# Kernel tuning notes

Measured on AMD Instinct MI355X. Metric: run time of the kernel, lower is better.

The kernel has to match this reference:

```python
import jax, jax.numpy as jnp
import numpy as np

B, T, S = 4, 2048, 512
HID, ND, NH = 2048, 1024, 16
HD = HID // NH  # 128
GATING_INIT = -4.0


def setup_inputs() -> dict:
    key = jax.random.key(0)
    ks = jax.random.split(key, 12)
    sc_h = 1.0 / np.sqrt(HID)
    sc_n = 1.0 / np.sqrt(ND)
    mask = jax.random.bernoulli(ks[2], 0.9, (B, S))
    mask = mask.at[:, 0].set(True)  # avoid fully-masked rows (NaN softmax)
    return {
        "hidden_states": jax.random.normal(ks[0], (B, T, HID), jnp.float32),
        "notes": jax.random.normal(ks[1], (B, S, ND), jnp.float32),
        "notes_mask": mask,
        "q_w": jax.random.normal(ks[3], (HID, HID), jnp.float32) * sc_h,
        "q_b": jax.random.normal(ks[4], (HID,), jnp.float32) * 0.01,
        "k_w": jax.random.normal(ks[5], (HID, ND), jnp.float32) * sc_n,
        "k_b": jax.random.normal(ks[6], (HID,), jnp.float32) * 0.01,
        "v_w": jax.random.normal(ks[7], (HID, ND), jnp.float32) * sc_n,
        "v_b": jax.random.normal(ks[8], (HID,), jnp.float32) * 0.01,
        "o_w": jax.random.normal(ks[9], (HID, HID), jnp.float32) * sc_h,
        "o_b": jax.random.normal(ks[10], (HID,), jnp.float32) * 0.01,
        "gate": jnp.full((1,), GATING_INIT, jnp.float32),
    }


def reference(hidden_states, notes, notes_mask, q_w, q_b, k_w, k_b, v_w, v_b, o_w, o_b, gate):
    # projections (torch Linear: x @ W^T + b)
    q = hidden_states @ q_w.T + q_b            # (B,T,HID)
    k = notes @ k_w.T + k_b                    # (B,S,HID)
    v = notes @ v_w.T + v_b                    # (B,S,HID)
    q = q.reshape(B, T, NH, HD).transpose(0, 2, 1, 3)  # (B,H,T,D)
    k = k.reshape(B, S, NH, HD).transpose(0, 2, 1, 3)  # (B,H,S,D)
    v = v.reshape(B, S, NH, HD).transpose(0, 2, 1, 3)
    scores = jnp.einsum("bhtd,bhsd->bhts", q, k) / jnp.sqrt(jnp.float32(HD))
    scores = jnp.where(notes_mask[:, None, None, :], scores, -jnp.inf)
    attn = jax.nn.softmax(scores, axis=-1)
    context = jnp.einsum("bhts,bhsd->bhtd", attn, v)   # (B,H,T,D)
    g = jax.nn.sigmoid(gate).reshape(1, 1, 1, 1)
    context = (g * context).transpose(0, 2, 1, 3).reshape(B, T, HID)
    delta = context @ o_w.T + o_b
    return delta
```

## Files before the change

kernel.cpp:

```cpp
#include <hip/hip_runtime.h>
#include <hip/hip_bf16.h>
#include <stdint.h>

#define B_ 4
#define T_ 2048
#define S_ 512
#define HID_ 2048
#define ND_ 1024
#define NH_ 16
#define HD_ 128

typedef unsigned short u16;
typedef unsigned int u32;
typedef __attribute__((ext_vector_type(8))) short bf16x8;
typedef __attribute__((ext_vector_type(4))) float f32x4;
typedef __attribute__((ext_vector_type(16))) float f32x16;
typedef __attribute__((ext_vector_type(4))) float f4;
typedef __attribute__((ext_vector_type(4))) u16 us4;
typedef __attribute__((ext_vector_type(8))) u16 us8;
typedef __attribute__((ext_vector_type(4))) u32 u32x4;

__device__ inline u16 f2bf(float f) {
  unsigned u = __builtin_bit_cast(unsigned, f);
  u += 0x7FFFu + ((u >> 16) & 1u);
  return (u16)(u >> 16);
}

__device__ inline u32 cvtpk(float lo, float hi) {
  u32 r;
  asm("v_cvt_pk_bf16_f32 %0, %1, %2" : "=v"(r) : "v"(lo), "v"(hi));
  return r;
}

__device__ inline f32x4 mfma16(bf16x8 a, bf16x8 b, f32x4 c) {
  return __builtin_amdgcn_mfma_f32_16x16x32_bf16(a, b, c, 0, 0, 0);
}
__device__ inline f32x16 mfma32(bf16x8 a, bf16x8 b, f32x16 c) {
  return __builtin_amdgcn_mfma_f32_32x32x16_bf16(a, b, c, 0, 0, 0);
}

__device__ inline void gload_lds16(const u16* g, u16* l) {
  __builtin_amdgcn_global_load_lds(
      (const __attribute__((address_space(1))) unsigned int*)g,
      (__attribute__((address_space(3))) unsigned int*)l, 16, 0, 0);
}

__global__ __launch_bounds__(256) void convert_all(
    const float* __restrict__ h, const float* __restrict__ n,
    const float* __restrict__ qw, const float* __restrict__ kw,
    const float* __restrict__ vw, const float* __restrict__ ow,
    u16* __restrict__ dh, u16* __restrict__ dn, u16* __restrict__ dqw,
    u16* __restrict__ dkw, u16* __restrict__ dvw, u16* __restrict__ dow) {
  const int C0 = 4194304;
  const int C1 = C0 + 524288;
  const int C2 = C1 + 1048576;
  const int C3 = C2 + 524288;
  const int C4 = C3 + 524288;
  const int C5 = C4 + 1048576;
  for (int c = blockIdx.x * blockDim.x + threadIdx.x; c < C5;
       c += gridDim.x * blockDim.x) {
    const float* s; u16* d; int o;
    if (c < C0)      { s = h;  d = dh;  o = c; }
    else if (c < C1) { s = n;  d = dn;  o = c - C0; }
    else if (c < C2) { s = qw; d = dqw; o = c - C1; }
    else if (c < C3) { s = kw; d = dkw; o = c - C2; }
    else if (c < C4) { s = vw; d = dvw; o = c - C3; }
    else             { s = ow; d = dow; o = c - C4; }
    f4 v = ((const f4*)s)[o];
    us4 r = { f2bf(v[0]), f2bf(v[1]), f2bf(v[2]), f2bf(v[3]) };
    ((us4*)d)[o] = r;
  }
}

template <bool OUT_BF16>
__global__ __launch_bounds__(256) void gemm_bt(
    const u16* __restrict__ A, const u16* __restrict__ Bm,
    const float* __restrict__ bias, void* __restrict__ Cout,
    int M, int N, int K) {
  __shared__ u16 As[128 * 32];
  __shared__ u16 Bs[128 * 32];
  const int tid = threadIdx.x;
  const int lane = tid & 63;
  const int wave = tid >> 6;
  const int wr = (wave >> 1) * 64;
  const int wc = (wave & 1) * 64;
  const int c15 = lane & 15;
  const int g = lane >> 4;
  const int bx = blockIdx.x, by = blockIdx.y;

  const u16* gA = A + (size_t)(by * 128 + (tid >> 2)) * K + (tid & 3) * 8;
  const u16* gB = Bm + (size_t)(bx * 128 + (tid >> 2)) * K + (tid & 3) * 8;

  f32x4 acc[4][4];
#pragma unroll
  for (int i = 0; i < 4; ++i)
#pragma unroll
    for (int j = 0; j < 4; ++j) acc[i][j] = (f32x4){0.f, 0.f, 0.f, 0.f};

  for (int k0 = 0; k0 < K; k0 += 32) {
    gload_lds16(gA + k0, &As[wave * 512]);
    gload_lds16(gA + (size_t)64 * K + k0, &As[2048 + wave * 512]);
    gload_lds16(gB + k0, &Bs[wave * 512]);
    gload_lds16(gB + (size_t)64 * K + k0, &Bs[2048 + wave * 512]);
    __syncthreads();
    bf16x8 af[4], bfr[4];
#pragma unroll
    for (int mt = 0; mt < 4; ++mt)
      af[mt] = *(const bf16x8*)&As[(wr + mt * 16 + c15) * 32 + g * 8];
#pragma unroll
    for (int nt = 0; nt < 4; ++nt)
      bfr[nt] = *(const bf16x8*)&Bs[(wc + nt * 16 + c15) * 32 + g * 8];
#pragma unroll
    for (int mt = 0; mt < 4; ++mt)
#pragma unroll
      for (int nt = 0; nt < 4; ++nt)
        acc[mt][nt] = mfma16(af[mt], bfr[nt], acc[mt][nt]);
    __syncthreads();
  }

#pragma unroll
  for (int mt = 0; mt < 4; ++mt)
#pragma unroll
    for (int nt = 0; nt < 4; ++nt) {
      const int m = by * 128 + wr + mt * 16 + g * 4;
      const int n = bx * 128 + wc + nt * 16 + c15;
      const float bv = bias[n];
#pragma unroll
      for (int r = 0; r < 4; ++r) {
        const float v = acc[mt][nt][r] + bv;
        if (OUT_BF16)
          ((u16*)Cout)[(size_t)(m + r) * N + n] = f2bf(v);
        else
          ((float*)Cout)[(size_t)(m + r) * N + n] = v;
      }
    }
}

template <bool OUT_BF16>
__global__ __launch_bounds__(512, 2) void gemm_pipe(
    const u16* __restrict__ A, const u16* __restrict__ Bm,
    const float* __restrict__ bias, void* __restrict__ Cout,
    int M, int N, int K) {
  extern __shared__ u16 lds[];
  const int tid = threadIdx.x;
  const int lane = tid & 63, wave = tid >> 6;
  const int wm = wave >> 2, wn = wave & 3;
  const int c15 = lane & 15, g = lane >> 4;
  const int bid = blockIdx.y * gridDim.x + blockIdx.x;
  const int sw = (bid & 7) * 32 + (bid >> 3);
  const int bn = sw & 7, bm = sw >> 3;
  const int NT = K >> 5;

  const int srow = tid >> 2;
  const int sx = (tid & 3) ^ ((srow >> 1) & 3);
  const u16* pa0 = A + (size_t)(bm * 256 + srow) * K + sx * 8;
  const u16* pa1 = A + (size_t)(bm * 256 + 128 + srow) * K + sx * 8;
  const u16* pb0 = Bm + (size_t)(bn * 256 + srow) * K + sx * 8;
  const u16* pb1 = Bm + (size_t)(bn * 256 + 128 + srow) * K + sx * 8;

  const int xr = (c15 >> 1) & 3;
  const int aoff = wm * 4096 + c15 * 32 + (g ^ xr) * 8;
  const int boff = 8192 + wn * 2048 + c15 * 32 + (g ^ xr) * 8;

  f32x4 acc[8][4];
#pragma unroll
  for (int i = 0; i < 8; ++i)
#pragma unroll
    for (int j = 0; j < 4; ++j) acc[i][j] = (f32x4){0.f, 0.f, 0.f, 0.f};

  {
    u16* sA = lds + wave * 512;
    u16* sB = lds + 8192 + wave * 512;
    gload_lds16(pa0, sA);          gload_lds16(pa1, sA + 4096);
    gload_lds16(pb0, sB);          gload_lds16(pb1, sB + 4096);
    pa0 += 32; pa1 += 32; pb0 += 32; pb1 += 32;
    gload_lds16(pa0, sA + 16384);  gload_lds16(pa1, sA + 20480);
    gload_lds16(pb0, sB + 16384);  gload_lds16(pb1, sB + 20480);
    pa0 += 32; pa1 += 32; pb0 += 32; pb1 += 32;
  }
  asm volatile("s_waitcnt vmcnt(4)" ::: "memory");
  __builtin_amdgcn_s_barrier();

  for (int t = 0; t < NT; ++t) {
    const bool more = (t + 2 < NT);
    const u16* cb = lds + (t & 3) * 16384;
    u16* sb = lds + ((t + 2) & 3) * 16384;

    bf16x8 a[8], b[4];
#pragma unroll
    for (int mf = 0; mf < 4; ++mf)
      a[mf] = *(const bf16x8*)(cb + aoff + mf * 512);
#pragma unroll
    for (int nf = 0; nf < 4; ++nf)
      b[nf] = *(const bf16x8*)(cb + boff + nf * 512);
#pragma unroll
    for (int mf = 4; mf < 8; ++mf)
      a[mf] = *(const bf16x8*)(cb + aoff + mf * 512);

    if (more) {
      gload_lds16(pa0, sb + wave * 512);
      gload_lds16(pa1, sb + 4096 + wave * 512);
      gload_lds16(pb0, sb + 8192 + wave * 512);
      gload_lds16(pb1, sb + 12288 + wave * 512);
      pa0 += 32; pa1 += 32; pb0 += 32; pb1 += 32;
    }

    __builtin_amdgcn_s_setprio(1);
#pragma unroll
    for (int mf = 0; mf < 8; ++mf)
#pragma unroll
      for (int nf = 0; nf < 4; ++nf)
        acc[mf][nf] = mfma16(a[mf], b[nf], acc[mf][nf]);
    __builtin_amdgcn_s_setprio(0);

    if (more) asm volatile("s_waitcnt vmcnt(4)" ::: "memory");
    else      asm volatile("s_waitcnt vmcnt(0)" ::: "memory");
    __builtin_amdgcn_s_barrier();
  }

#pragma unroll
  for (int mf = 0; mf < 8; ++mf)
#pragma unroll
    for (int nf = 0; nf < 4; ++nf) {
      const int m = bm * 256 + wm * 128 + mf * 16 + g * 4;
      const int n = bn * 256 + wn * 64 + nf * 16 + c15;
      const float bv = bias[n];
#pragma unroll
      for (int r = 0; r < 4; ++r) {
        const float v = acc[mf][nf][r] + bv;
        if (OUT_BF16)
          ((u16*)Cout)[(size_t)(m + r) * N + n] = f2bf(v);
        else
          ((float*)Cout)[(size_t)(m + r) * N + n] = v;
      }
    }
}

__global__ __launch_bounds__(256) void transpose_v(const u16* __restrict__ v,
                                                   u16* __restrict__ vt) {
  __shared__ u16 tile[32][36];
  const int s0 = blockIdx.x * 32;
  const int bh = blockIdx.y;
  const int d0 = blockIdx.z * 32;
  const int b = bh >> 4, h = bh & 15;
  const int tid = threadIdx.x;
  const int sl = tid >> 3, dl = (tid & 7) * 4;
  us4 val = *(const us4*)(v + (size_t)(b * S_ + s0 + sl) * HID_ + h * HD_ + d0 + dl);
  *(us4*)&tile[sl][dl] = val;
  __syncthreads();
  const int dl2 = tid >> 3, sl2 = (tid & 7) * 4;
  us4 outv = { tile[sl2 + 0][dl2], tile[sl2 + 1][dl2],
               tile[sl2 + 2][dl2], tile[sl2 + 3][dl2] };
  *(us4*)(vt + ((size_t)bh * HD_ + d0 + dl2) * S_ + s0 + sl2) = outv;
}

__global__ __launch_bounds__(256) void attn_fwd(
    const u16* __restrict__ q, const u16* __restrict__ k,
    const u16* __restrict__ vt, const int* __restrict__ mask,
    const float* __restrict__ gate, u16* __restrict__ ctx) {
  __shared__ u16 smem[17408];
  __shared__ float addend[S_];
  const int tid = threadIdx.x, lane = tid & 63, wave = tid >> 6;
  const int bh = blockIdx.y, b = bh >> 4, h = bh & 15;
  const int tw = blockIdx.x * 128 + wave * 32;
  const int l31 = lane & 31, hi = lane >> 5;

  const u16* kb  = k + (size_t)b * S_ * HID_ + h * HD_;
  const u16* vtb = vt + (size_t)bh * HD_ * S_;

  const u16* sp[4];
  int dj[4];
  u16* ldsbase;
  ptrdiff_t stride;
  if (wave < 2) {
    ldsbase = smem;
    stride = 32 * HID_;
#pragma unroll
    for (int i = 0; i < 4; ++i) {
      const int jj = wave * 4 + i;
      const int row = jj * 4 + (lane >> 4);
      const int cb = (lane & 15) * 16;
      const int cbp = cb ^ ((row & 7) << 4);
      sp[i] = kb + (size_t)row * HID_ + (cbp >> 1);
      dj[i] = jj * 512;
    }
  } else {
    ldsbase = smem + 8192;
    stride = 32;
#pragma unroll
    for (int i = 0; i < 4; ++i) {
      const int jj = (wave - 2) * 4 + i;
      const int d = jj * 16 + (lane >> 2);
      const int cb = (lane & 3) * 16;
      const int cbp = cb ^ ((d & 3) << 4);
      sp[i] = vtb + (size_t)d * S_ + (cbp >> 1);
      dj[i] = jj * 512;
    }
  }
#define STAGE(cur)                                            \
  do {                                                        \
    _Pragma("unroll") for (int i_ = 0; i_ < 4; ++i_) {        \
      gload_lds16(sp[i_], ldsbase + (cur) * 4096 + dj[i_]);   \
      sp[i_] += stride;                                       \
    }                                                         \
  } while (0)

  STAGE(0);

  for (int s = tid; s < S_; s += 256)
    addend[s] = mask[b * S_ + s] ? 0.f : -1e30f;

  const u16* qrow = q + (size_t)(b * T_ + tw + l31) * HID_ + h * HD_;
  bf16x8 qf[8];
#pragma unroll
  for (int dc = 0; dc < 8; ++dc)
    qf[dc] = *(const bf16x8*)&qrow[dc * 16 + hi * 8];

  int kofs[8];
#pragma unroll
  for (int dc = 0; dc < 8; ++dc)
    kofs[dc] = l31 * 128 + (((dc * 32 + hi * 16) ^ ((l31 & 7) << 4)) >> 1);
  const int vcol0 = ((hi * 16) ^ ((l31 & 3) << 4)) >> 1;
  const int vcol1 = ((32 + hi * 16) ^ ((l31 & 3) << 4)) >> 1;

  float m_run = -1e30f, l_run = 0.f;
  f32x16 ct[4];
#pragma unroll
  for (int i = 0; i < 4; ++i)
#pragma unroll
    for (int r = 0; r < 16; ++r) ct[i][r] = 0.f;
  const float scale = 0.08838834764831845f;

  __syncthreads();

  for (int it = 0; it < 16; ++it) {
    const int cur = it & 1;
    if (it < 15) STAGE(cur ^ 1);
    const int s0 = it * 32;
    const u16* kt = smem + cur * 4096;
    const u16* vl = smem + 8192 + cur * 4096;

    f32x16 st;
#pragma unroll
    for (int r = 0; r < 16; ++r) st[r] = 0.f;
    __builtin_amdgcn_s_setprio(1);
#pragma unroll
    for (int dc = 0; dc < 8; ++dc) {
      bf16x8 kf = *(const bf16x8*)&kt[kofs[dc]];
      st = mfma32(kf, qf[dc], st);
    }
    __builtin_amdgcn_s_setprio(0);

    float sc[16];
#pragma unroll
    for (int rq = 0; rq < 4; ++rq) {
      f4 ad = *(const f4*)&addend[s0 + rq * 8 + hi * 4];
#pragma unroll
      for (int m = 0; m < 4; ++m)
        sc[rq * 4 + m] = st[rq * 4 + m] * scale + ad[m];
    }
    float tm = sc[0];
#pragma unroll
    for (int i = 1; i < 16; ++i) tm = fmaxf(tm, sc[i]);
    tm = fmaxf(tm, __shfl_xor(tm, 32));
    const float nm = fmaxf(m_run, tm);
    if (!__all(nm - m_run <= 8.f)) {
      const float corr = __expf(m_run - nm);
      l_run *= corr;
#pragma unroll
      for (int db = 0; db < 4; ++db)
#pragma unroll
        for (int r = 0; r < 16; ++r) ct[db][r] *= corr;
      m_run = nm;
    }
    float p[16], ps = 0.f;
#pragma unroll
    for (int i = 0; i < 16; ++i) { p[i] = __expf(sc[i] - m_run); ps += p[i]; }
    ps += __shfl_xor(ps, 32);
    l_run += ps;

    u32 w[8], x[8];
#pragma unroll
    for (int q2 = 0; q2 < 4; ++q2) {
      w[2 * q2]     = cvtpk(p[4 * q2],     p[4 * q2 + 1]);
      w[2 * q2 + 1] = cvtpk(p[4 * q2 + 2], p[4 * q2 + 3]);
    }
#pragma unroll
    for (int i = 0; i < 8; ++i) x[i] = __shfl_xor((int)w[i], 32);
    const u32x4 f0 = hi ? (u32x4){x[2], x[3], w[2], w[3]}
                        : (u32x4){w[0], w[1], x[0], x[1]};
    const u32x4 f1 = hi ? (u32x4){x[6], x[7], w[6], w[7]}
                        : (u32x4){w[4], w[5], x[4], x[5]};
    const bf16x8 pf0 = __builtin_bit_cast(bf16x8, f0);
    const bf16x8 pf1 = __builtin_bit_cast(bf16x8, f1);

    __builtin_amdgcn_s_setprio(1);
#pragma unroll
    for (int db = 0; db < 4; ++db) {
      bf16x8 vf0 = *(const bf16x8*)&vl[db * 1024 + l31 * 32 + vcol0];
      ct[db] = mfma32(vf0, pf0, ct[db]);
      bf16x8 vf1 = *(const bf16x8*)&vl[db * 1024 + l31 * 32 + vcol1];
      ct[db] = mfma32(vf1, pf1, ct[db]);
    }
    __builtin_amdgcn_s_setprio(0);

    __syncthreads();
  }
#undef STAGE

  const float gsig = 1.f / (1.f + __expf(-gate[0]));
  const float inv = gsig / l_run;
  u16* c_lds = smem + wave * 4352;
#pragma unroll
  for (int db = 0; db < 4; ++db)
#pragma unroll
    for (int rq = 0; rq < 4; ++rq) {
      us4 o = { f2bf(ct[db][rq * 4 + 0] * inv), f2bf(ct[db][rq * 4 + 1] * inv),
                f2bf(ct[db][rq * 4 + 2] * inv), f2bf(ct[db][rq * 4 + 3] * inv) };
      *(us4*)&c_lds[l31 * 136 + db * 32 + rq * 8 + hi * 4] = o;
    }
  u16* crow = ctx + (size_t)(b * T_ + tw) * HID_ + h * HD_;
#pragma unroll
  for (int rep = 0; rep < 8; ++rep) {
    const int tt = (lane >> 4) + rep * 4;
    us8 valv = *(const us8*)&c_lds[tt * 136 + (lane & 15) * 8];
    *(us8*)&crow[(size_t)tt * HID_ + (lane & 15) * 8] = valv;
  }
}

extern "C" void kernel_launch(void* const* d_in, const int* in_sizes, int n_in,
                              void* d_out, int out_size, void* d_ws, size_t ws_size,
                              hipStream_t stream) {
  (void)in_sizes; (void)n_in; (void)out_size; (void)ws_size;
  const float* hs   = (const float*)d_in[0];
  const float* nts  = (const float*)d_in[1];
  const int*   mask = (const int*)d_in[2];
  const float* qw   = (const float*)d_in[3];
  const float* qb   = (const float*)d_in[4];
  const float* kw   = (const float*)d_in[5];
  const float* kbi  = (const float*)d_in[6];
  const float* vw   = (const float*)d_in[7];
  const float* vbi  = (const float*)d_in[8];
  const float* ow   = (const float*)d_in[9];
  const float* obi  = (const float*)d_in[10];
  const float* gate = (const float*)d_in[11];
  float* out = (float*)d_out;

  char* w = (char*)d_ws;
  u16* h_bf   = (u16*)(w + 0);
  u16* n_bf   = (u16*)(w + 33554432);
  u16* qw_bf  = (u16*)(w + 37748736);
  u16* kw_bf  = (u16*)(w + 46137344);
  u16* vw_bf  = (u16*)(w + 50331648);
  u16* ow_bf  = (u16*)(w + 54525952);
  u16* q_bf   = (u16*)(w + 62914560);
  u16* k_bf   = (u16*)(w + 96468992);
  u16* v_bf   = (u16*)(w + 104857600);
  u16* vt_bf  = (u16*)(w + 113246208);
  u16* ctx_bf = h_bf;

  hipFuncSetAttribute(reinterpret_cast<const void*>(&gemm_pipe<true>),
                      hipFuncAttributeMaxDynamicSharedMemorySize, 131072);
  hipFuncSetAttribute(reinterpret_cast<const void*>(&gemm_pipe<false>),
                      hipFuncAttributeMaxDynamicSharedMemorySize, 131072);

  convert_all<<<dim3(2048), dim3(256), 0, stream>>>(
      hs, nts, qw, kw, vw, ow, h_bf, n_bf, qw_bf, kw_bf, vw_bf, ow_bf);
  gemm_bt<true><<<dim3(16, 16), dim3(256), 0, stream>>>(
      n_bf, kw_bf, kbi, k_bf, 2048, 2048, 1024);
  gemm_bt<true><<<dim3(16, 16), dim3(256), 0, stream>>>(
      n_bf, vw_bf, vbi, v_bf, 2048, 2048, 1024);
  transpose_v<<<dim3(16, 64, 4), dim3(256), 0, stream>>>(v_bf, vt_bf);
  gemm_pipe<true><<<dim3(8, 32), dim3(512), 131072, stream>>>(
      h_bf, qw_bf, qb, q_bf, 8192, 2048, 2048);
  attn_fwd<<<dim3(16, 64), dim3(256), 0, stream>>>(
      q_bf, k_bf, vt_bf, mask, gate, ctx_bf);
  gemm_pipe<false><<<dim3(8, 32), dim3(512), 131072, stream>>>(
      ctx_bf, ow_bf, obi, out, 8192, 2048, 2048);
}
```

Measured before the change: 280.8 us.

## Software-pipeline LDS fragment loads across k-steps in the projection GEMM loop

Restructures the GEMM main loop so the low-half A fragments and the B fragments for step t+1 are read from LDS right after the barrier. These reads overlap with the second half of the MFMAs for step t, and the loop is unrolled by two with double-buffered registers. Global-to-LDS loads are split into two halves placed around the first MFMA block. The aim is to hide LDS read latency behind matrix math. The cost is higher register pressure, and the loop relies on NT being even.

```diff
diff --git a/kernel.cpp b/kernel.cpp
--- a/kernel.cpp
+++ b/kernel.cpp
@@ -181,41 +181,60 @@
   asm volatile("s_waitcnt vmcnt(4)" ::: "memory");
   __builtin_amdgcn_s_barrier();
 
-  for (int t = 0; t < NT; ++t) {
-    const bool more = (t + 2 < NT);
-    const u16* cb = lds + (t & 3) * 16384;
-    u16* sb = lds + ((t + 2) & 3) * 16384;
-
-    bf16x8 a[8], b[4];
-#pragma unroll
-    for (int mf = 0; mf < 4; ++mf)
-      a[mf] = *(const bf16x8*)(cb + aoff + mf * 512);
-#pragma unroll
-    for (int nf = 0; nf < 4; ++nf)
-      b[nf] = *(const bf16x8*)(cb + boff + nf * 512);
-#pragma unroll
-    for (int mf = 4; mf < 8; ++mf)
-      a[mf] = *(const bf16x8*)(cb + aoff + mf * 512);
-
-    if (more) {
-      gload_lds16(pa0, sb + wave * 512);
-      gload_lds16(pa1, sb + 4096 + wave * 512);
-      gload_lds16(pb0, sb + 8192 + wave * 512);
-      gload_lds16(pb1, sb + 12288 + wave * 512);
-      pa0 += 32; pa1 += 32; pb0 += 32; pb1 += 32;
-    }
-
-    __builtin_amdgcn_s_setprio(1);
-#pragma unroll
-    for (int mf = 0; mf < 8; ++mf)
-#pragma unroll
-      for (int nf = 0; nf < 4; ++nf)
-        acc[mf][nf] = mfma16(a[mf], b[nf], acc[mf][nf]);
-    __builtin_amdgcn_s_setprio(0);
-
-    if (more) asm volatile("s_waitcnt vmcnt(4)" ::: "memory");
-    else      asm volatile("s_waitcnt vmcnt(0)" ::: "memory");
-    __builtin_amdgcn_s_barrier();
+  bf16x8 aLo[2][4], bF[2][4], aHi[4];
+#pragma unroll
+  for (int i = 0; i < 4; ++i) {
+    aLo[0][i] = *(const bf16x8*)(lds + aoff + i * 512);
+    bF[0][i]  = *(const bf16x8*)(lds + boff + i * 512);
+  }
+
+  for (int tt = 0; tt < NT; tt += 2) {
+#pragma unroll
+    for (int ph = 0; ph < 2; ++ph) {
+      const int t = tt + ph;
+      const bool more = (t + 2 < NT);
+      const bool nxt  = (t + 1 < NT);
+      const u16* cb = lds + ((t & 3) << 14);
+      u16* sb = lds + (((t + 2) & 3) << 14);
+
+#pragma unroll
+      for (int i = 0; i < 4; ++i)
+        aHi[i] = *(const bf16x8*)(cb + aoff + (4 + i) * 512);
+      if (more) {
+        gload_lds16(pa0, sb + wave * 512);
+        gload_lds16(pa1, sb + 4096 + wave * 512);
+      }
+      __builtin_amdgcn_s_setprio(1);
+#pragma unroll
+      for (int mf = 0; mf < 4; ++mf)
+#pragma unroll
+        for (int nf = 0; nf < 4; ++nf)
+          acc[mf][nf] = mfma16(aLo[ph][mf], bF[ph][nf], acc[mf][nf]);
+      __builtin_amdgcn_s_setprio(0);
+      if (more) {
+        gload_lds16(pb0, sb + 8192 + wave * 512);
+        gload_lds16(pb1, sb + 12288 + wave * 512);
+        pa0 += 32; pa1 += 32; pb0 += 32; pb1 += 32;
+      }
+      if (more) asm volatile("s_waitcnt vmcnt(4)" ::: "memory");
+      else      asm volatile("s_waitcnt vmcnt(0)" ::: "memory");
+      __builtin_amdgcn_s_barrier();
+      if (nxt) {
+        const u16* nb = lds + (((t + 1) & 3) << 14);
+#pragma unroll
+        for (int i = 0; i < 4; ++i) {
+          aLo[ph ^ 1][i] = *(const bf16x8*)(nb + aoff + i * 512);
+          bF[ph ^ 1][i]  = *(const bf16x8*)(nb + boff + i * 512);
+        }
+      }
+      __builtin_amdgcn_s_setprio(1);
+#pragma unroll
+      for (int mf = 0; mf < 4; ++mf)
+#pragma unroll
+        for (int nf = 0; nf < 4; ++nf)
+          acc[4 + mf][nf] = mfma16(aHi[mf], bF[ph][nf], acc[4 + mf][nf]);
+      __builtin_amdgcn_s_setprio(0);
+    }
   }
 
 #pragma unroll
```

Result: no change. 281.5 us (+0.2%).

## Restructure big GEMM into 8-phase ping-pong pipeline with 64-wide K tiles

Applied to the files above, without the earlier changes.

Replaces the 4-stage 32-wide K loop of the large Q and output GEMMs with a double-buffered 64-wide K tile. Each iteration is split into four MFMA quadrant phases, with barriers between them, and the global-to-LDS loads for the next tile's sub-blocks are interleaved between those phases. LDS uses a new XOR swizzle. The aim is to hide LDS reads and global loads behind MFMA work and cut loop overhead, in the style of an 8-wave ping-pong schedule. It adds many more barriers per iteration and relies on the vmcnt accounting being correct.

```diff
diff --git a/kernel.cpp b/kernel.cpp
--- a/kernel.cpp
+++ b/kernel.cpp
@@ -137,7 +137,7 @@
 }
 
 template <bool OUT_BF16>
-__global__ __launch_bounds__(512, 2) void gemm_pipe(
+__global__ __launch_bounds__(512, 2) void gemm8p(
     const u16* __restrict__ A, const u16* __restrict__ Bm,
     const float* __restrict__ bias, void* __restrict__ Cout,
     int M, int N, int K) {
@@ -149,18 +149,26 @@
   const int bid = blockIdx.y * gridDim.x + blockIdx.x;
   const int sw = (bid & 7) * 32 + (bid >> 3);
   const int bn = sw & 7, bm = sw >> 3;
-  const int NT = K >> 5;
-
-  const int srow = tid >> 2;
-  const int sx = (tid & 3) ^ ((srow >> 1) & 3);
-  const u16* pa0 = A + (size_t)(bm * 256 + srow) * K + sx * 8;
-  const u16* pa1 = A + (size_t)(bm * 256 + 128 + srow) * K + sx * 8;
-  const u16* pb0 = Bm + (size_t)(bn * 256 + srow) * K + sx * 8;
-  const u16* pb1 = Bm + (size_t)(bn * 256 + 128 + srow) * K + sx * 8;
-
-  const int xr = (c15 >> 1) & 3;
-  const int aoff = wm * 4096 + c15 * 32 + (g ^ xr) * 8;
-  const int boff = 8192 + wn * 2048 + c15 * 32 + (g ^ xr) * 8;
+  const int NT = K >> 6;
+
+  const int r0 = wave * 8 + (lane >> 3);
+  const int scol = ((lane & 7) * 16) ^ ((lane >> 5) << 5);
+  const size_t dK = (size_t)64 * K;
+  const u16* pAlo = A + (size_t)(bm * 256 + r0) * K + (scol >> 1);
+  const u16* pAhi = A + (size_t)(bm * 256 + 128 + r0) * K + (scol >> 1);
+  const u16* pBlo = Bm + (size_t)(bn * 256 + r0) * K + (scol >> 1);
+  const u16* pBhi = Bm + (size_t)(bn * 256 + 128 + r0) * K + (scol >> 1);
+
+#define STG(p, dst)                                  \
+  do {                                               \
+    gload_lds16((p), (dst) + wave * 512);            \
+    gload_lds16((p) + dK, (dst) + 4096 + wave * 512);\
+    (p) += 64;                                       \
+  } while (0)
+
+  const int sg = (g * 8) ^ ((c15 & 4) << 2);
+  const int aoff = wm * 8192 + c15 * 64 + sg;
+  const int boff = 16384 + (wn >> 1) * 8192 + (wn & 1) * 4096 + c15 * 64 + sg;
 
   f32x4 acc[8][4];
 #pragma unroll
@@ -168,55 +176,102 @@
 #pragma unroll
     for (int j = 0; j < 4; ++j) acc[i][j] = (f32x4){0.f, 0.f, 0.f, 0.f};
 
-  {
-    u16* sA = lds + wave * 512;
-    u16* sB = lds + 8192 + wave * 512;
-    gload_lds16(pa0, sA);          gload_lds16(pa1, sA + 4096);
-    gload_lds16(pb0, sB);          gload_lds16(pb1, sB + 4096);
-    pa0 += 32; pa1 += 32; pb0 += 32; pb1 += 32;
-    gload_lds16(pa0, sA + 16384);  gload_lds16(pa1, sA + 20480);
-    gload_lds16(pb0, sB + 16384);  gload_lds16(pb1, sB + 20480);
-    pa0 += 32; pa1 += 32; pb0 += 32; pb1 += 32;
+  STG(pAlo, lds);
+  STG(pAhi, lds + 8192);
+  STG(pBlo, lds + 16384);
+  STG(pBhi, lds + 24576);
+  STG(pAlo, lds + 32768);
+  asm volatile("s_waitcnt vmcnt(2)" ::: "memory");
+  __builtin_amdgcn_s_barrier();
+
+  for (int j = 0; j < NT; ++j) {
+    const int cu = (j & 1) << 15;
+    const u16* cb = lds + cu;
+    u16* nb = lds + (cu ^ 32768);
+    const bool s1 = (j + 1 < NT);
+    const bool s2 = (j + 2 < NT);
+
+    bf16x8 aL[4][2], bL[2][2];
+#pragma unroll
+    for (int fm = 0; fm < 4; ++fm)
+#pragma unroll
+      for (int h = 0; h < 2; ++h)
+        aL[fm][h] = *(const bf16x8*)(cb + aoff + fm * 1024 + h * 32);
+#pragma unroll
+    for (int fn = 0; fn < 2; ++fn)
+#pragma unroll
+      for (int h = 0; h < 2; ++h)
+        bL[fn][h] = *(const bf16x8*)(cb + boff + fn * 1024 + h * 32);
+    if (s1) STG(pAhi, nb + 8192);
+    __builtin_amdgcn_s_barrier();
+    asm volatile("s_waitcnt lgkmcnt(0)" ::: "memory");
+    __builtin_amdgcn_s_setprio(1);
+#pragma unroll
+    for (int fm = 0; fm < 4; ++fm)
+#pragma unroll
+      for (int fn = 0; fn < 2; ++fn) {
+        acc[fm][fn] = mfma16(aL[fm][0], bL[fn][0], acc[fm][fn]);
+        acc[fm][fn] = mfma16(aL[fm][1], bL[fn][1], acc[fm][fn]);
+      }
+    __builtin_amdgcn_s_setprio(0);
+    __builtin_amdgcn_s_barrier();
+
+    bf16x8 bH[2][2];
+#pragma unroll
+    for (int fn = 0; fn < 2; ++fn)
+#pragma unroll
+      for (int h = 0; h < 2; ++h)
+        bH[fn][h] = *(const bf16x8*)(cb + boff + (2 + fn) * 1024 + h * 32);
+    if (s1) STG(pBlo, nb + 16384);
+    __builtin_amdgcn_s_barrier();
+    asm volatile("s_waitcnt lgkmcnt(0)" ::: "memory");
+    __builtin_amdgcn_s_setprio(1);
+#pragma unroll
+    for (int fm = 0; fm < 4; ++fm)
+#pragma unroll
+      for (int fn = 0; fn < 2; ++fn) {
+        acc[fm][2 + fn] = mfma16(aL[fm][0], bH[fn][0], acc[fm][2 + fn]);
+        acc[fm][2 + fn] = mfma16(aL[fm][1], bH[fn][1], acc[fm][2 + fn]);
+      }
+    __builtin_amdgcn_s_setprio(0);
+    __builtin_amdgcn_s_barrier();
+
+    bf16x8 aH[4][2];
+#pragma unroll
+    for (int fm = 0; fm < 4; ++fm)
+#pragma unroll
+      for (int h = 0; h < 2; ++h)
+        aH[fm][h] = *(const bf16x8*)(cb + aoff + (4 + fm) * 1024 + h * 32);
+    if (s1) STG(pBhi, nb + 24576);
+    __builtin_amdgcn_sched_barrier(0);
+    if (s2) STG(pAlo, lds + cu);
+    __builtin_amdgcn_s_barrier();
+    asm volatile("s_waitcnt lgkmcnt(0)" ::: "memory");
+    __builtin_amdgcn_s_setprio(1);
+#pragma unroll
+    for (int fm = 0; fm < 4; ++fm)
+#pragma unroll
+      for (int fn = 0; fn < 2; ++fn) {
+        acc[4 + fm][2 + fn] = mfma16(aH[fm][0], bH[fn][0], acc[4 + fm][2 + fn]);
+        acc[4 + fm][2 + fn] = mfma16(aH[fm][1], bH[fn][1], acc[4 + fm][2 + fn]);
+      }
+    __builtin_amdgcn_s_setprio(0);
+    __builtin_amdgcn_s_barrier();
+
+    __builtin_amdgcn_s_setprio(1);
+#pragma unroll
+    for (int fm = 0; fm < 4; ++fm)
+#pragma unroll
+      for (int fn = 0; fn < 2; ++fn) {
+        acc[4 + fm][fn] = mfma16(aH[fm][0], bL[fn][0], acc[4 + fm][fn]);
+        acc[4 + fm][fn] = mfma16(aH[fm][1], bL[fn][1], acc[4 + fm][fn]);
+      }
+    __builtin_amdgcn_s_setprio(0);
+    if (s2) asm volatile("s_waitcnt vmcnt(2)" ::: "memory");
+    else    asm volatile("s_waitcnt vmcnt(0)" ::: "memory");
+    __builtin_amdgcn_s_barrier();
   }
-  asm volatile("s_waitcnt vmcnt(4)" ::: "memory");
-  __builtin_amdgcn_s_barrier();
-
-  for (int t = 0; t < NT; ++t) {
-    const bool more = (t + 2 < NT);
-    const u16* cb = lds + (t & 3) * 16384;
-    u16* sb = lds + ((t + 2) & 3) * 16384;
-
-    bf16x8 a[8], b[4];
-#pragma unroll
-    for (int mf = 0; mf < 4; ++mf)
-      a[mf] = *(const bf16x8*)(cb + aoff + mf * 512);
-#pragma unroll
-    for (int nf = 0; nf < 4; ++nf)
-      b[nf] = *(const bf16x8*)(cb + boff + nf * 512);
-#pragma unroll
-    for (int mf = 4; mf < 8; ++mf)
-      a[mf] = *(const bf16x8*)(cb + aoff + mf * 512);
-
-    if (more) {
-      gload_lds16(pa0, sb + wave * 512);
-      gload_lds16(pa1, sb + 4096 + wave * 512);
-      gload_lds16(pb0, sb + 8192 + wave * 512);
-      gload_lds16(pb1, sb + 12288 + wave * 512);
-      pa0 += 32; pa1 += 32; pb0 += 32; pb1 += 32;
-    }
-
-    __builtin_amdgcn_s_setprio(1);
-#pragma unroll
-    for (int mf = 0; mf < 8; ++mf)
-#pragma unroll
-      for (int nf = 0; nf < 4; ++nf)
-        acc[mf][nf] = mfma16(a[mf], b[nf], acc[mf][nf]);
-    __builtin_amdgcn_s_setprio(0);
-
-    if (more) asm volatile("s_waitcnt vmcnt(4)" ::: "memory");
-    else      asm volatile("s_waitcnt vmcnt(0)" ::: "memory");
-    __builtin_amdgcn_s_barrier();
-  }
+#undef STG
 
 #pragma unroll
   for (int mf = 0; mf < 8; ++mf)
@@ -459,9 +514,9 @@
   u16* vt_bf  = (u16*)(w + 113246208);
   u16* ctx_bf = h_bf;
 
-  hipFuncSetAttribute(reinterpret_cast<const void*>(&gemm_pipe<true>),
+  hipFuncSetAttribute(reinterpret_cast<const void*>(&gemm8p<true>),
                       hipFuncAttributeMaxDynamicSharedMemorySize, 131072);
-  hipFuncSetAttribute(reinterpret_cast<const void*>(&gemm_pipe<false>),
+  hipFuncSetAttribute(reinterpret_cast<const void*>(&gemm8p<false>),
                       hipFuncAttributeMaxDynamicSharedMemorySize, 131072);
 
   convert_all<<<dim3(2048), dim3(256), 0, stream>>>(
@@ -471,10 +526,10 @@
   gemm_bt<true><<<dim3(16, 16), dim3(256), 0, stream>>>(
       n_bf, vw_bf, vbi, v_bf, 2048, 2048, 1024);
   transpose_v<<<dim3(16, 64, 4), dim3(256), 0, stream>>>(v_bf, vt_bf);
-  gemm_pipe<true><<<dim3(8, 32), dim3(512), 131072, stream>>>(
+  gemm8p<true><<<dim3(8, 32), dim3(512), 131072, stream>>>(
       h_bf, qw_bf, qb, q_bf, 8192, 2048, 2048);
   attn_fwd<<<dim3(16, 64), dim3(256), 0, stream>>>(
       q_bf, k_bf, vt_bf, mask, gate, ctx_bf);
-  gemm_pipe<false><<<dim3(8, 32), dim3(512), 131072, stream>>>(
+  gemm8p<false><<<dim3(8, 32), dim3(512), 131072, stream>>>(
       ctx_bf, ow_bf, obi, out, 8192, 2048, 2048);
 }
```

Result: no change. 284.7 us (+1.4%).
